# Optimization experiments

Measured on AMD Instinct MI355X. Metric: run time of the kernel, lower is better.

## Reference

```python
import jax, jax.numpy as jnp
import numpy as np

IN_C = 128
OUT_C = 128
N_NODES = 50000
N_EDGES = 500000


def setup_inputs() -> dict:
    key = jax.random.key(0)
    ks = jax.random.split(key, 12)
    s = lambda k, shp, fan: jax.random.normal(k, shp, jnp.float32) * (1.0 / np.sqrt(fan))
    return {
        "node_embeddings": jax.random.normal(ks[0], (N_NODES, IN_C), jnp.float32),
        "edge_index": jax.random.randint(ks[1], (2, N_EDGES), 0, N_NODES, jnp.int64),
        # source_proj / target_proj: Linear(in, in)
        "Ws": s(ks[2], (IN_C, IN_C), IN_C), "bs": jnp.zeros((IN_C,), jnp.float32),
        "Wt": s(ks[3], (IN_C, IN_C), IN_C), "bt": jnp.zeros((IN_C,), jnp.float32),
        # attention_mlp: Linear(2in, in) -> ReLU -> Linear(in, 1) -> Sigmoid
        "Wa1": s(ks[4], (2 * IN_C, IN_C), 2 * IN_C), "ba1": jnp.zeros((IN_C,), jnp.float32),
        "Wa2": s(ks[5], (IN_C, 1), IN_C), "ba2": jnp.zeros((1,), jnp.float32),
        # edge_mlp: Linear(2in, 2out) -> GeGLU -> LayerNorm(out)
        "We": s(ks[6], (2 * IN_C, 2 * OUT_C), 2 * IN_C), "be": jnp.zeros((2 * OUT_C,), jnp.float32),
        "gamma": jnp.ones((OUT_C,), jnp.float32), "beta": jnp.zeros((OUT_C,), jnp.float32),
    }


def reference(node_embeddings, edge_index, Ws, bs, Wt, bt, Wa1, ba1, Wa2, ba2, We, be, gamma, beta):
    # gather + dual projection  -> [E, in], [E, in]
    src = node_embeddings[edge_index[0]] @ Ws + bs
    tgt = node_embeddings[edge_index[1]] @ Wt + bt
    edge_features = jnp.concatenate([src, tgt], axis=-1)  # [E, 2*in]
    # sigmoid attention gate  -> [E, 1]
    h = jax.nn.relu(edge_features @ Wa1 + ba1)
    attn = jax.nn.sigmoid(h @ Wa2 + ba2)
    attended = edge_features * attn  # [E, 2*in]
    # edge MLP: Linear -> GeGLU -> LayerNorm
    z = attended @ We + be  # [E, 2*out]
    x, gate = jnp.split(z, 2, axis=-1)
    g = x * jax.nn.gelu(gate, approximate=False)  # [E, out]
    mu = jnp.mean(g, axis=-1, keepdims=True)
    var = jnp.var(g, axis=-1, keepdims=True)
    out = (g - mu) * jax.lax.rsqrt(var + 1e-5) * gamma + beta
    return out
```

## Files before the change

### kernel.cpp

```cpp
#include <hip/hip_runtime.h>
#include <hip/hip_bf16.h>


typedef __bf16 bf16x8 __attribute__((ext_vector_type(8)));
typedef float f32x4 __attribute__((ext_vector_type(4)));

__device__ __forceinline__ unsigned short f2b(float f) {
    unsigned int u = __float_as_uint(f);
    unsigned int r = (u + 0x7fffu + ((u >> 16) & 1u)) >> 16;
    return (unsigned short)r;
}

__global__ __launch_bounds__(256) void pack_weights(
    const float* __restrict__ Ws, const float* __restrict__ Wt,
    const float* __restrict__ Wa1, const float* __restrict__ We,
    unsigned short* __restrict__ Wp1, unsigned short* __restrict__ Wp2)
{
    int id = blockIdx.x * 256 + threadIdx.x;
    if (id < 32768) {
        int n = id >> 7, k = id & 127;
        float v = (n < 128) ? Ws[k * 128 + n] : Wt[k * 128 + (n - 128)];
        Wp1[id] = f2b(v);
    }
    if (id < 98304) {
        int n = id >> 8, k = id & 255;
        float v = (n < 128) ? Wa1[k * 128 + n] : We[k * 256 + (n - 128)];
        Wp2[id] = f2b(v);
    }
}

__global__ __launch_bounds__(256) void node_proj(
    const float* __restrict__ emb, const unsigned short* __restrict__ Wp1,
    const float* __restrict__ bs, const float* __restrict__ bt,
    unsigned short* __restrict__ P, int NN)
{
    __shared__ unsigned short Alds[16][136];
    int t = threadIdx.x;
    {
        int row = t >> 4, cp = (t & 15) * 8;
        int node = blockIdx.x * 16 + row;
        if (node >= NN) node = NN - 1;
        const float* sp = emb + (size_t)node * 128 + cp;
        float4 v0 = *(const float4*)sp;
        float4 v1 = *(const float4*)(sp + 4);
        union { uint4 u; unsigned short s[8]; } pk;
        pk.s[0] = f2b(v0.x); pk.s[1] = f2b(v0.y); pk.s[2] = f2b(v0.z); pk.s[3] = f2b(v0.w);
        pk.s[4] = f2b(v1.x); pk.s[5] = f2b(v1.y); pk.s[6] = f2b(v1.z); pk.s[7] = f2b(v1.w);
        *(uint4*)&Alds[row][cp] = pk.u;
    }
    __syncthreads();
    int wv = t >> 6, lane = t & 63, n15 = lane & 15, quad = lane >> 4;
    f32x4 z4 = {0.f, 0.f, 0.f, 0.f};
    f32x4 acc[4] = {z4, z4, z4, z4};
    for (int ks = 0; ks < 4; ++ks) {
        bf16x8 a = *(const bf16x8*)&Alds[n15][ks * 32 + quad * 8];
#pragma unroll
        for (int tl = 0; tl < 4; ++tl) {
            int n = (wv * 4 + tl) * 16 + n15;
            bf16x8 b = *(const bf16x8*)(Wp1 + n * 128 + ks * 32 + quad * 8);
            acc[tl] = __builtin_amdgcn_mfma_f32_16x16x32_bf16(a, b, acc[tl], 0, 0, 0);
        }
    }
#pragma unroll
    for (int tl = 0; tl < 4; ++tl) {
        int c = (wv * 4 + tl) * 16 + n15;
        float bias = (c < 128) ? bs[c] : bt[c - 128];
#pragma unroll
        for (int r = 0; r < 4; ++r) {
            int node = blockIdx.x * 16 + quad * 4 + r;
            if (node < NN) P[(size_t)node * 256 + c] = f2b(acc[tl][r] + bias);
        }
    }
}

__global__ __launch_bounds__(256, 3) void edge_kernel(
    const int* __restrict__ eidx, const unsigned short* __restrict__ P,
    const unsigned short* __restrict__ Wp2,
    const float* __restrict__ ba1, const float* __restrict__ Wa2,
    const float* __restrict__ ba2, const float* __restrict__ be,
    const float* __restrict__ gamma, const float* __restrict__ beta,
    float* __restrict__ out, int E)
{
    __shared__ unsigned short Alds[64][264];
    __shared__ float attnP[4][64];
    __shared__ float lnP[4][2][64];
    int t = threadIdx.x;
    int base = blockIdx.x * 64;

#pragma unroll
    for (int i = 0; i < 8; ++i) {
        int c = t + i * 256;
        int e = c >> 5, p = c & 31;
        int ge = base + e; if (ge >= E) ge = E - 1;
        int node = (p < 16) ? eidx[ge] : eidx[E + ge];
        *(uint4*)&Alds[e][p * 8] = *(const uint4*)(P + (size_t)node * 256 + p * 8);
    }
    __syncthreads();

    int wv = t >> 6, lane = t & 63, n15 = lane & 15, quad = lane >> 4;
    f32x4 z4 = {0.f, 0.f, 0.f, 0.f};
    const unsigned short* wbase = Wp2 + (size_t)(wv * 16 + n15) * 256 + quad * 8;

    f32x4 acc1[8];
#pragma unroll
    for (int i = 0; i < 8; ++i) acc1[i] = z4;
    for (int ks = 0; ks < 8; ++ks) {
        bf16x8 a[4];
#pragma unroll
        for (int m = 0; m < 4; ++m)
            a[m] = *(const bf16x8*)&Alds[m * 16 + n15][ks * 32 + quad * 8];
#pragma unroll
        for (int n = 0; n < 2; ++n) {
            bf16x8 b = *(const bf16x8*)(wbase + n * 16384 + ks * 32);
#pragma unroll
            for (int m = 0; m < 4; ++m)
                acc1[n * 4 + m] = __builtin_amdgcn_mfma_f32_16x16x32_bf16(a[m], b, acc1[n * 4 + m], 0, 0, 0);
        }
    }

    float ba2s = ba2[0];
    float ba1v[2], wa2v[2];
#pragma unroll
    for (int n = 0; n < 2; ++n) {
        int col = (wv + 4 * n) * 16 + n15;
        ba1v[n] = ba1[col]; wa2v[n] = Wa2[col];
    }
#pragma unroll
    for (int m = 0; m < 4; ++m) {
#pragma unroll
        for (int r = 0; r < 4; ++r) {
            float v = fmaxf(acc1[m][r] + ba1v[0], 0.f) * wa2v[0]
                    + fmaxf(acc1[4 + m][r] + ba1v[1], 0.f) * wa2v[1];
            v += __shfl_xor(v, 1); v += __shfl_xor(v, 2);
            v += __shfl_xor(v, 4); v += __shfl_xor(v, 8);
            if (n15 == m * 4 + r) attnP[wv][m * 16 + quad * 4 + r] = v;
        }
    }
    __syncthreads();

    float attn[4][4];
#pragma unroll
    for (int m = 0; m < 4; ++m) {
#pragma unroll
        for (int r = 0; r < 4; ++r) {
            int row = m * 16 + quad * 4 + r;
            float s = attnP[0][row] + attnP[1][row] + attnP[2][row] + attnP[3][row];
            attn[m][r] = 1.f / (1.f + expf(-(s + ba2s)));
        }
    }

    f32x4 acc2[16];
#pragma unroll
    for (int i = 0; i < 16; ++i) acc2[i] = z4;
    for (int ks = 0; ks < 8; ++ks) {
        bf16x8 a[4];
#pragma unroll
        for (int m = 0; m < 4; ++m)
            a[m] = *(const bf16x8*)&Alds[m * 16 + n15][ks * 32 + quad * 8];
#pragma unroll
        for (int j = 0; j < 4; ++j) {
            bf16x8 b = *(const bf16x8*)(wbase + (2 + j) * 16384 + ks * 32);
#pragma unroll
            for (int m = 0; m < 4; ++m)
                acc2[j * 4 + m] = __builtin_amdgcn_mfma_f32_16x16x32_bf16(a[m], b, acc2[j * 4 + m], 0, 0, 0);
        }
    }

    float bex[2], beg[2], gmv[2], btv[2];
#pragma unroll
    for (int j = 0; j < 2; ++j) {
        int col = wv * 16 + j * 64 + n15;
        bex[j] = be[col];       beg[j] = be[128 + col];
        gmv[j] = gamma[col];    btv[j] = beta[col];
    }
#pragma unroll
    for (int m = 0; m < 4; ++m) {
#pragma unroll
        for (int r = 0; r < 4; ++r) {
            float s1 = 0.f, s2 = 0.f;
#pragma unroll
            for (int j = 0; j < 2; ++j) {
                float zx = fmaf(attn[m][r], acc2[j * 4 + m][r], bex[j]);
                float zg = fmaf(attn[m][r], acc2[(2 + j) * 4 + m][r], beg[j]);
                float g = zx * (0.5f * zg * (1.f + erff(zg * 0.70710678118f)));
                acc2[j * 4 + m][r] = g;
                s1 += g; s2 = fmaf(g, g, s2);
            }
            s1 += __shfl_xor(s1, 1); s1 += __shfl_xor(s1, 2);
            s1 += __shfl_xor(s1, 4); s1 += __shfl_xor(s1, 8);
            s2 += __shfl_xor(s2, 1); s2 += __shfl_xor(s2, 2);
            s2 += __shfl_xor(s2, 4); s2 += __shfl_xor(s2, 8);
            if (n15 == m * 4 + r) {
                lnP[wv][0][m * 16 + quad * 4 + r] = s1;
                lnP[wv][1][m * 16 + quad * 4 + r] = s2;
            }
        }
    }
    __syncthreads();

    float* Olds = (float*)Alds;
#pragma unroll
    for (int m = 0; m < 4; ++m) {
#pragma unroll
        for (int r = 0; r < 4; ++r) {
            int row = m * 16 + quad * 4 + r;
            float s1 = lnP[0][0][row] + lnP[1][0][row] + lnP[2][0][row] + lnP[3][0][row];
            float s2 = lnP[0][1][row] + lnP[1][1][row] + lnP[2][1][row] + lnP[3][1][row];
            float mu = s1 * 0.0078125f;
            float var = s2 * 0.0078125f - mu * mu;
            float rs = rsqrtf(var + 1e-5f);
            Olds[row * 132 + wv * 16 + n15]      = (acc2[m][r]     - mu) * rs * gmv[0] + btv[0];
            Olds[row * 132 + 64 + wv * 16 + n15] = (acc2[4 + m][r] - mu) * rs * gmv[1] + btv[1];
        }
    }
    __syncthreads();

#pragma unroll
    for (int i = 0; i < 8; ++i) {
        int e = i * 8 + (t >> 5);
        int edge = base + e;
        if (edge < E) {
            int c = (t & 31) * 4;
            *(float4*)(out + (size_t)edge * 128 + c) = *(const float4*)&Olds[e * 132 + c];
        }
    }
}

extern "C" void kernel_launch(void* const* d_in, const int* in_sizes, int n_in,
                              void* d_out, int out_size, void* d_ws, size_t ws_size,
                              hipStream_t stream) {
    const float* emb  = (const float*)d_in[0];
    const int*   eidx = (const int*)d_in[1];
    const float* Ws   = (const float*)d_in[2];
    const float* bs   = (const float*)d_in[3];
    const float* Wt   = (const float*)d_in[4];
    const float* bt   = (const float*)d_in[5];
    const float* Wa1  = (const float*)d_in[6];
    const float* ba1  = (const float*)d_in[7];
    const float* Wa2  = (const float*)d_in[8];
    const float* ba2  = (const float*)d_in[9];
    const float* We   = (const float*)d_in[10];
    const float* be   = (const float*)d_in[11];
    const float* gam  = (const float*)d_in[12];
    const float* bet  = (const float*)d_in[13];
    float* out = (float*)d_out;
    int NN = in_sizes[0] / 128;
    int E  = in_sizes[1] / 2;
    unsigned short* Wp1 = (unsigned short*)d_ws;
    unsigned short* Wp2 = Wp1 + 32768;
    unsigned short* P   = Wp2 + 98304;
    hipLaunchKernelGGL(pack_weights, dim3(384), dim3(256), 0, stream,
                       Ws, Wt, Wa1, We, Wp1, Wp2);
    hipLaunchKernelGGL(node_proj, dim3((NN + 15) / 16), dim3(256), 0, stream,
                       emb, Wp1, bs, bt, P, NN);
    hipLaunchKernelGGL(edge_kernel, dim3((E + 63) / 64), dim3(256), 0, stream,
                       eidx, P, Wp2, ba1, Wa2, ba2, be, gam, bet, out, E);
}
```

Before: 571.6 us.

## Retile node projection to 64 rows, stage output in LDS, use fast erf/sigmoid

The node projection kernel now processes 64 nodes per block instead of 16. Each weight fragment is reused across four row tiles, and the bf16 outputs are staged through shared memory so they can be written back with coalesced 16-byte stores. In the edge kernel, the sigmoid switches to __expf/__fdividef and the exact erff in GELU is replaced by an Abramowitz-Stegun polynomial approximation. This trades some numerical accuracy in GELU (max error around 1e-7 in erf) for fewer instructions in the edge epilogue.

New measurement: 551.7 us. 3.5% less time.

```diff
diff --git a/kernel.cpp b/kernel.cpp
--- a/kernel.cpp
+++ b/kernel.cpp
@@ -9,6 +9,16 @@
     unsigned int u = __float_as_uint(f);
     unsigned int r = (u + 0x7fffu + ((u >> 16) & 1u)) >> 16;
     return (unsigned short)r;
+}
+
+__device__ __forceinline__ float erf_fast(float x) {
+    float ax = __builtin_fabsf(x);
+    float t = __fdividef(1.f, fmaf(0.3275911f, ax, 1.f));
+    float y = t * fmaf(t, fmaf(t, fmaf(t, fmaf(t, 1.061405429f, -1.453152027f),
+                                       1.421413741f), -0.284496736f), 0.254829592f);
+    float e = __expf(-ax * ax);
+    float r = fmaf(-y, e, 1.f);
+    return __builtin_copysignf(r, x);
 }
 
 __global__ __launch_bounds__(256) void pack_weights(
@@ -34,41 +44,67 @@
     const float* __restrict__ bs, const float* __restrict__ bt,
     unsigned short* __restrict__ P, int NN)
 {
-    __shared__ unsigned short Alds[16][136];
+    __shared__ __align__(16) unsigned short SH[64 * 264];
     int t = threadIdx.x;
-    {
-        int row = t >> 4, cp = (t & 15) * 8;
-        int node = blockIdx.x * 16 + row;
-        if (node >= NN) node = NN - 1;
+    int base = blockIdx.x * 64;
+
+#pragma unroll
+    for (int i = 0; i < 4; ++i) {
+        int c = t + i * 256;
+        int row = c >> 4, cp = (c & 15) * 8;
+        int node = base + row; if (node >= NN) node = NN - 1;
         const float* sp = emb + (size_t)node * 128 + cp;
         float4 v0 = *(const float4*)sp;
         float4 v1 = *(const float4*)(sp + 4);
         union { uint4 u; unsigned short s[8]; } pk;
         pk.s[0] = f2b(v0.x); pk.s[1] = f2b(v0.y); pk.s[2] = f2b(v0.z); pk.s[3] = f2b(v0.w);
         pk.s[4] = f2b(v1.x); pk.s[5] = f2b(v1.y); pk.s[6] = f2b(v1.z); pk.s[7] = f2b(v1.w);
-        *(uint4*)&Alds[row][cp] = pk.u;
-    }
-    __syncthreads();
+        *(uint4*)&SH[row * 136 + cp] = pk.u;
+    }
+    __syncthreads();
+
     int wv = t >> 6, lane = t & 63, n15 = lane & 15, quad = lane >> 4;
     f32x4 z4 = {0.f, 0.f, 0.f, 0.f};
-    f32x4 acc[4] = {z4, z4, z4, z4};
+    f32x4 acc[16];
+#pragma unroll
+    for (int i = 0; i < 16; ++i) acc[i] = z4;
+
+    const unsigned short* wbase = Wp1 + (size_t)(wv * 16 + n15) * 128 + quad * 8;
     for (int ks = 0; ks < 4; ++ks) {
-        bf16x8 a = *(const bf16x8*)&Alds[n15][ks * 32 + quad * 8];
-#pragma unroll
-        for (int tl = 0; tl < 4; ++tl) {
-            int n = (wv * 4 + tl) * 16 + n15;
-            bf16x8 b = *(const bf16x8*)(Wp1 + n * 128 + ks * 32 + quad * 8);
-            acc[tl] = __builtin_amdgcn_mfma_f32_16x16x32_bf16(a, b, acc[tl], 0, 0, 0);
-        }
-    }
-#pragma unroll
-    for (int tl = 0; tl < 4; ++tl) {
-        int c = (wv * 4 + tl) * 16 + n15;
-        float bias = (c < 128) ? bs[c] : bt[c - 128];
-#pragma unroll
-        for (int r = 0; r < 4; ++r) {
-            int node = blockIdx.x * 16 + quad * 4 + r;
-            if (node < NN) P[(size_t)node * 256 + c] = f2b(acc[tl][r] + bias);
+        bf16x8 a[4];
+#pragma unroll
+        for (int m = 0; m < 4; ++m)
+            a[m] = *(const bf16x8*)&SH[(m * 16 + n15) * 136 + ks * 32 + quad * 8];
+#pragma unroll
+        for (int k = 0; k < 4; ++k) {
+            bf16x8 b = *(const bf16x8*)(wbase + k * 8192 + ks * 32);
+#pragma unroll
+            for (int m = 0; m < 4; ++m)
+                acc[k * 4 + m] = __builtin_amdgcn_mfma_f32_16x16x32_bf16(a[m], b, acc[k * 4 + m], 0, 0, 0);
+        }
+    }
+    __syncthreads();
+
+#pragma unroll
+    for (int k = 0; k < 4; ++k) {
+        int colk = (wv + 4 * k) * 16 + n15;
+        float bias = (colk < 128) ? bs[colk] : bt[colk - 128];
+#pragma unroll
+        for (int m = 0; m < 4; ++m) {
+#pragma unroll
+            for (int r = 0; r < 4; ++r)
+                SH[(m * 16 + quad * 4 + r) * 264 + colk] = f2b(acc[k * 4 + m][r] + bias);
+        }
+    }
+    __syncthreads();
+
+#pragma unroll
+    for (int i = 0; i < 8; ++i) {
+        int e = i * 8 + (t >> 5);
+        int node = base + e;
+        if (node < NN) {
+            int c = (t & 31) * 8;
+            *(uint4*)(P + (size_t)node * 256 + c) = *(const uint4*)&SH[e * 264 + c];
         }
     }
 }
@@ -145,7 +181,7 @@
         for (int r = 0; r < 4; ++r) {
             int row = m * 16 + quad * 4 + r;
             float s = attnP[0][row] + attnP[1][row] + attnP[2][row] + attnP[3][row];
-            attn[m][r] = 1.f / (1.f + expf(-(s + ba2s)));
+            attn[m][r] = __fdividef(1.f, 1.f + __expf(-(s + ba2s)));
         }
     }
 
@@ -182,7 +218,7 @@
             for (int j = 0; j < 2; ++j) {
                 float zx = fmaf(attn[m][r], acc2[j * 4 + m][r], bex[j]);
                 float zg = fmaf(attn[m][r], acc2[(2 + j) * 4 + m][r], beg[j]);
-                float g = zx * (0.5f * zg * (1.f + erff(zg * 0.70710678118f)));
+                float g = zx * (0.5f * zg * (1.f + erf_fast(zg * 0.70710678118f)));
                 acc2[j * 4 + m][r] = g;
                 s1 += g; s2 = fmaf(g, g, s2);
             }
@@ -251,7 +287,7 @@
     unsigned short* P   = Wp2 + 98304;
     hipLaunchKernelGGL(pack_weights, dim3(384), dim3(256), 0, stream,
                        Ws, Wt, Wa1, We, Wp1, Wp2);
-    hipLaunchKernelGGL(node_proj, dim3((NN + 15) / 16), dim3(256), 0, stream,
+    hipLaunchKernelGGL(node_proj, dim3((NN + 63) / 64), dim3(256), 0, stream,
                        emb, Wp1, bs, bt, P, NN);
     hipLaunchKernelGGL(edge_kernel, dim3((E + 63) / 64), dim3(256), 0, stream,
                        eidx, P, Wp2, ba1, Wa2, ba2, be, gam, bet, out, E);
```
